# Kernel tuning notes

Hardware: AMD Instinct MI355X
Metric: run time of the kernel (lower is better)

Reference implementation:

```python
import jax, jax.numpy as jnp
import numpy as np

N, E, D, ED = 50000, 800000, 64, 2


def setup_inputs() -> dict:
    key = jax.random.key(0)
    ks = jax.random.split(key, 16)
    inp = {
        "h": jax.random.normal(ks[0], (N, D), jnp.float32),
        "coord": jax.random.normal(ks[1], (N, 3), jnp.float32),
        "edge_index": jax.random.randint(ks[2], (2, E), 0, N, jnp.int32),
        "edge_attr": jax.random.normal(ks[3], (E, ED), jnp.float32),
        # edge_mlp: Linear(2D+1+ED -> D), Linear(D -> D)
        "W_e1": jax.random.normal(ks[4], (2 * D + 1 + ED, D), jnp.float32) * 0.08,
        "b_e1": jnp.zeros((D,), jnp.float32),
        "W_e2": jax.random.normal(ks[5], (D, D), jnp.float32) * 0.12,
        "b_e2": jnp.zeros((D,), jnp.float32),
        # node_mlp: Linear(D+D -> D), Linear(D -> D)
        "W_n1": jax.random.normal(ks[6], (2 * D, D), jnp.float32) * 0.08,
        "b_n1": jnp.zeros((D,), jnp.float32),
        "W_n2": jax.random.normal(ks[7], (D, D), jnp.float32) * 0.12,
        "b_n2": jnp.zeros((D,), jnp.float32),
        # coord_mlp: Linear(D -> D), Linear(D -> 1, bias=False, xavier gain 0.001)
        "W_c1": jax.random.normal(ks[8], (D, D), jnp.float32) * 0.12,
        "b_c1": jnp.zeros((D,), jnp.float32),
        "W_c2": jax.random.normal(ks[9], (D, 1), jnp.float32) * 1e-3,
    }
    return inp


def reference(h, coord, edge_index, edge_attr,
              W_e1, b_e1, W_e2, b_e2,
              W_n1, b_n1, W_n2, b_n2,
              W_c1, b_c1, W_c2):
    row, col = edge_index[0], edge_index[1]
    n_nodes = h.shape[0]

    # coord2radial
    coord_diff = coord[row] - coord[col]                       # [E,3]
    radial = jnp.sum(coord_diff * coord_diff, axis=-1, keepdims=True)  # [E,1]

    # edge_model
    e_in = jnp.concatenate([h[row], h[col], radial, edge_attr], axis=-1)  # [E, 2D+1+ED]
    e = jax.nn.silu(e_in @ W_e1 + b_e1)
    edge_feat = jax.nn.silu(e @ W_e2 + b_e2)                   # [E,D]

    # coord_model: trans = coord_diff * coord_mlp(edge_feat), clamp, segment mean
    scale = jax.nn.silu(edge_feat @ W_c1 + b_c1) @ W_c2        # [E,1]
    trans = jnp.clip(coord_diff * scale, -100.0, 100.0)        # [E,3]
    agg_c = jax.ops.segment_sum(trans, row, num_segments=n_nodes)       # [N,3]
    cnt = jax.ops.segment_sum(jnp.ones((trans.shape[0],), trans.dtype), row,
                              num_segments=n_nodes)            # [N]
    coord_out = coord + agg_c / jnp.clip(cnt, 1.0, None)[:, None]  # coords_weight=1.0

    # node_model: segment sum of edge_feat by row, node MLP, residual
    agg_h = jax.ops.segment_sum(edge_feat, row, num_segments=n_nodes)   # [N,D]
    n_in = jnp.concatenate([h, agg_h], axis=-1)                # [N,2D]
    h_out = h + (jax.nn.silu(n_in @ W_n1 + b_n1) @ W_n2 + b_n2)

    return (h_out, coord_out)
```

## Files before the change

kernel.cpp:

```cpp
#include <hip/hip_runtime.h>

#define DD 64
#define NTE 512
#define SLOTMAX 64

using s8v   = __attribute__((ext_vector_type(8))) short;
using f32x4 = __attribute__((ext_vector_type(4))) float;

typedef unsigned int   uint_t;
typedef unsigned short ushort_t;

union U8 { s8v v; uint_t u[4]; };

__device__ __forceinline__ float silu_f(float x) {
    return x / (1.0f + __expf(-x));
}
__device__ __forceinline__ float clamp100(float x) {
    return fminf(fmaxf(x, -100.0f), 100.0f);
}
__device__ __forceinline__ unsigned short f2bf(float x) {
    unsigned int u = __float_as_uint(x);
    return (unsigned short)((u + 0x7FFFu + ((u >> 16) & 1u)) >> 16);
}
__device__ __forceinline__ uint_t cvt_pk_bf16(float lo, float hi) {
    uint_t r;
    asm("v_cvt_pk_bf16_f32 %0, %1, %2" : "=v"(r) : "v"(lo), "v"(hi));
    return r;
}

#define WAVE_FENCE() do { asm volatile("s_waitcnt lgkmcnt(0)" ::: "memory"); \
                          __builtin_amdgcn_sched_barrier(0); } while (0)

__global__ __launch_bounds__(256) void prep_all(
    const float* __restrict__ h,
    const float* __restrict__ coord,
    const float* __restrict__ We1, const float* __restrict__ We2,
    const float* __restrict__ Wc1,
    const float* __restrict__ Wn1, const float* __restrict__ Wn2,
    const float* __restrict__ be1, const float* __restrict__ be2,
    const float* __restrict__ bc1,
    const int*   __restrict__ ei,
    ushort_t* __restrict__ hbf,
    ushort_t* __restrict__ wf,
    float4* __restrict__ coord4,
    int* __restrict__ cnt_i,
    int2* __restrict__ slots2,
    int N, int E, int total8, int histBlocks, int hbfBlocks, int c4Blocks)
{
    const int b = blockIdx.x;
    if (b < histBlocks) {
        const int e = b * 256 + threadIdx.x;
        if (e < E) {
            const int r = ei[e];
            const int s = atomicAdd(&cnt_i[r], 1);
            if (s < SLOTMAX) {
                int2 v; v.x = e; v.y = ei[E + e];
                slots2[(size_t)r * SLOTMAX + s] = v;
            }
        }
    } else if (b < histBlocks + hbfBlocks) {
        const int t = (b - histBlocks) * 256 + threadIdx.x;
        if (t < total8) {
            const float4 v0 = ((const float4*)h)[t * 2 + 0];
            const float4 v1 = ((const float4*)h)[t * 2 + 1];
            uint4 o;
            o.x = (uint_t)f2bf(v0.x) | ((uint_t)f2bf(v0.y) << 16);
            o.y = (uint_t)f2bf(v0.z) | ((uint_t)f2bf(v0.w) << 16);
            o.z = (uint_t)f2bf(v1.x) | ((uint_t)f2bf(v1.y) << 16);
            o.w = (uint_t)f2bf(v1.z) | ((uint_t)f2bf(v1.w) << 16);
            ((uint4*)hbf)[t] = o;
        }
    } else if (b < histBlocks + hbfBlocks + c4Blocks) {
        const int t = (b - histBlocks - hbfBlocks) * 256 + threadIdx.x;
        if (t < N) {
            float4 c;
            c.x = coord[3 * t + 0];
            c.y = coord[3 * t + 1];
            c.z = coord[3 * t + 2];
            c.w = 0.0f;
            coord4[t] = c;
        }
    } else {
        const int t = (b - histBlocks - hbfBlocks - c4Blocks) * 256 + threadIdx.x;
        if (t >= 32768) return;
        if (t < 28672) {
            const int j    = t & 7;
            const int lane = (t >> 3) & 63;
            const int n0   = (t >> 9) & 3;
            const int k0   = (t >> 11) & 1;
            const int mat  = t >> 12;
            const int g    = lane >> 4;
            int k;
            if (mat == 2 || mat == 3) k = 16 * (2 * k0 + (j >> 2)) + 4 * g + (j & 3);
            else                      k = k0 * 32 + g * 8 + j;
            const int n = n0 * 16 + (lane & 15);
            float v;
            if      (mat == 0) v = We1[(size_t)k * 64 + n];
            else if (mat == 1) v = We1[(size_t)(64 + k) * 64 + n];
            else if (mat == 2) v = We2[(size_t)k * 64 + n];
            else if (mat == 3) v = Wc1[(size_t)k * 64 + n];
            else if (mat == 4) v = Wn1[(size_t)k * 64 + n];
            else if (mat == 5) v = Wn1[(size_t)(64 + k) * 64 + n];
            else               v = Wn2[(size_t)k * 64 + n];
            wf[t] = f2bf(v);
        } else {
            const int t2   = t - 28672;
            const int j    = t2 & 7;
            const int lane = (t2 >> 3) & 63;
            const int n0   = (t2 >> 9) & 3;
            const int xm   = (t2 >> 11) & 1;
            const int k = 8 * (lane >> 4) + j;
            const int m = n0 * 16 + (lane & 15);
            float v = 0.0f;
            if (xm == 0) {
                if      (k == 0) v = We1[(size_t)128 * 64 + m];
                else if (k == 1) v = We1[(size_t)129 * 64 + m];
                else if (k == 2) v = We1[(size_t)130 * 64 + m];
                else if (k == 3) v = be1[m];
            } else {
                if      (k == 0) v = be2[m];
                else if (k == 1) v = bc1[m];
            }
            wf[t] = f2bf(v);
        }
    }
}

__global__ __launch_bounds__(NTE, 4) void egcl_edge(
    const ushort_t* __restrict__ hbf,
    const ushort_t* __restrict__ wfG,
    const float4* __restrict__ coord4,
    const float* __restrict__ ea,
    const float* __restrict__ Wc2,
    const int* __restrict__ cnt_i,
    const int2* __restrict__ slots2,
    ushort_t* __restrict__ aggbf,
    float* __restrict__ coord_out,
    int N, int totalWaves)
{
    __shared__ ushort_t fragLDS[20480];

    const int tid = threadIdx.x;
    #pragma unroll
    for (int i = 0; i < 4; ++i)
        ((uint4*)fragLDS)[tid + i * 512] = ((const uint4*)wfG)[tid + i * 512];
    ((uint4*)fragLDS)[2048 + tid] = ((const uint4*)wfG)[3584 + tid];
    __syncthreads();

    const int wid  = tid >> 6;
    const int lane = tid & 63;
    const int l15  = lane & 15;
    const int g    = lane >> 4;

#define LD_W(mat, k0, m0) \
    (*(const s8v*)(fragLDS + ((((mat)*2 + (k0))*4 + (m0)) * 512) + lane * 8))
#define LD_X7(m0) (*(const s8v*)(fragLDS + 16384 + (m0) * 512 + lane * 8))
#define LD_XB(m0) (*(const s8v*)(fragLDS + 18432 + (m0) * 512 + lane * 8))

    float wc2_c[4][4];
    #pragma unroll
    for (int m0 = 0; m0 < 4; ++m0)
        #pragma unroll
        for (int j = 0; j < 4; ++j)
            wc2_c[m0][j] = Wc2[m0 * 16 + 4 * g + j];

    U8 b2f, bcf;
    b2f.u[0] = 0x00003F80u; b2f.u[1] = 0; b2f.u[2] = 0; b2f.u[3] = 0;
    bcf.u[0] = 0x3F800000u; bcf.u[1] = 0; bcf.u[2] = 0; bcf.u[3] = 0;

    const f32x4 zero4 = {0.f, 0.f, 0.f, 0.f};

    int n = blockIdx.x * 8 + wid;
    int pdeg = 0;
    int2 pslot; pslot.x = 0; pslot.y = 0;
    if (n < N) {
        pdeg  = cnt_i[n];
        pslot = slots2[(size_t)n * SLOTMAX + l15];
    }

    for (; n < N; n += totalWaves) {
        const int deg    = pdeg;
        const int2 slot0 = pslot;
        const int nn = n + totalWaves;
        if (nn < N) {
            pdeg  = cnt_i[nn];
            pslot = slots2[(size_t)nn * SLOTMAX + l15];
        }

        const int effdeg = deg < SLOTMAX ? deg : SLOTMAX;
        const float4 cn4 = coord4[n];
        const int s0x = __shfl(slot0.x, lane & 48, 64);
        const int s0y = __shfl(slot0.y, lane & 48, 64);

        const ushort_t* hn = hbf + (size_t)n * 64;
        const s8v bn0 = *(const s8v*)(hn + g * 8);
        const s8v bn1 = *(const s8v*)(hn + 32 + g * 8);
        f32x4 rowacc[4];
        #pragma unroll
        for (int m0 = 0; m0 < 4; ++m0) {
            f32x4 a = zero4;
            a = __builtin_amdgcn_mfma_f32_16x16x32_bf16(LD_W(0, 0, m0), bn0, a, 0, 0, 0);
            a = __builtin_amdgcn_mfma_f32_16x16x32_bf16(LD_W(0, 1, m0), bn1, a, 0, 0, 0);
            rowacc[m0] = a;
        }

        float hsum[4][4];
        #pragma unroll
        for (int m0 = 0; m0 < 4; ++m0)
            #pragma unroll
            for (int j = 0; j < 4; ++j) hsum[m0][j] = 0.f;
        float txs = 0.f, tys = 0.f, tzs = 0.f;

        const int ntile = (effdeg + 15) >> 4;
        int2 slNext; slNext.x = 0; slNext.y = 0;

        for (int t = 0; t < ntile; ++t) {
            const int s = t * 16 + l15;
            const bool val = (s < effdeg);
            const float valf = val ? 1.0f : 0.0f;

            int2 sl;
            if (t == 0) { sl.x = val ? slot0.x : s0x; sl.y = val ? slot0.y : s0y; }
            else        sl = slNext;

            if (t + 1 < ntile) {
                const int s2 = s + 16;
                slNext = slots2[(size_t)n * SLOTMAX + (s2 < effdeg ? s2 : 0)];
            }

            const float4 c4 = coord4[sl.y];
            const float2 a2 = *(const float2*)(ea + 2 * (size_t)sl.x);
            const ushort_t* hc = hbf + (size_t)sl.y * 64;
            const s8v bc0  = *(const s8v*)(hc + g * 8);
            const s8v bc1v = *(const s8v*)(hc + 32 + g * 8);

            const float dx = cn4.x - c4.x, dy = cn4.y - c4.y, dz = cn4.z - c4.z;
            const float radial = dx * dx + dy * dy + dz * dz;

            U8 ex;
            ex.u[0] = cvt_pk_bf16(radial, a2.x);
            ex.u[1] = cvt_pk_bf16(a2.y, 1.0f);
            ex.u[2] = 0; ex.u[3] = 0;

            f32x4 c1[4];
            #pragma unroll
            for (int m0 = 0; m0 < 4; ++m0) {
                f32x4 a = rowacc[m0];
                a = __builtin_amdgcn_mfma_f32_16x16x32_bf16(LD_W(1, 0, m0), bc0,  a, 0, 0, 0);
                a = __builtin_amdgcn_mfma_f32_16x16x32_bf16(LD_W(1, 1, m0), bc1v, a, 0, 0, 0);
                a = __builtin_amdgcn_mfma_f32_16x16x32_bf16(LD_X7(m0),      ex.v, a, 0, 0, 0);
                c1[m0] = a;
            }

            U8 f2a, f2b;
            #pragma unroll
            for (int m0 = 0; m0 < 4; ++m0) {
                const float ya = silu_f(c1[m0][0]);
                const float yb = silu_f(c1[m0][1]);
                const float yc = silu_f(c1[m0][2]);
                const float yd = silu_f(c1[m0][3]);
                U8& dst = (m0 < 2) ? f2a : f2b;
                dst.u[(m0 & 1) * 2 + 0] = cvt_pk_bf16(ya, yb);
                dst.u[(m0 & 1) * 2 + 1] = cvt_pk_bf16(yc, yd);
            }

            f32x4 c2[4];
            #pragma unroll
            for (int m0 = 0; m0 < 4; ++m0) {
                f32x4 a = zero4;
                a = __builtin_amdgcn_mfma_f32_16x16x32_bf16(LD_W(2, 0, m0), f2a.v, a, 0, 0, 0);
                a = __builtin_amdgcn_mfma_f32_16x16x32_bf16(LD_W(2, 1, m0), f2b.v, a, 0, 0, 0);
                a = __builtin_amdgcn_mfma_f32_16x16x32_bf16(LD_XB(m0),      b2f.v, a, 0, 0, 0);
                c2[m0] = a;
            }

            U8 f3a, f3b;
            #pragma unroll
            for (int m0 = 0; m0 < 4; ++m0) {
                const float ya = silu_f(c2[m0][0]);
                const float yb = silu_f(c2[m0][1]);
                const float yc = silu_f(c2[m0][2]);
                const float yd = silu_f(c2[m0][3]);
                hsum[m0][0] = fmaf(ya, valf, hsum[m0][0]);
                hsum[m0][1] = fmaf(yb, valf, hsum[m0][1]);
                hsum[m0][2] = fmaf(yc, valf, hsum[m0][2]);
                hsum[m0][3] = fmaf(yd, valf, hsum[m0][3]);
                U8& dst = (m0 < 2) ? f3a : f3b;
                dst.u[(m0 & 1) * 2 + 0] = cvt_pk_bf16(ya, yb);
                dst.u[(m0 & 1) * 2 + 1] = cvt_pk_bf16(yc, yd);
            }

            float p = 0.f;
            #pragma unroll
            for (int m0 = 0; m0 < 4; ++m0) {
                f32x4 a = zero4;
                a = __builtin_amdgcn_mfma_f32_16x16x32_bf16(LD_W(3, 0, m0), f3a.v, a, 0, 0, 0);
                a = __builtin_amdgcn_mfma_f32_16x16x32_bf16(LD_W(3, 1, m0), f3b.v, a, 0, 0, 0);
                a = __builtin_amdgcn_mfma_f32_16x16x32_bf16(LD_XB(m0),      bcf.v, a, 0, 0, 0);
                #pragma unroll
                for (int j = 0; j < 4; ++j)
                    p = fmaf(silu_f(a[j]), wc2_c[m0][j], p);
            }
            p += __shfl_xor(p, 16, 64);
            p += __shfl_xor(p, 32, 64);
            const float sc = p * valf;
            txs += clamp100(dx * sc);
            tys += clamp100(dy * sc);
            tzs += clamp100(dz * sc);
        }

        #pragma unroll
        for (int m0 = 0; m0 < 4; ++m0) {
            #pragma unroll
            for (int j = 0; j < 4; ++j) {
                float v = hsum[m0][j];
                v += __shfl_xor(v, 1, 64);
                v += __shfl_xor(v, 2, 64);
                v += __shfl_xor(v, 4, 64);
                v += __shfl_xor(v, 8, 64);
                hsum[m0][j] = v;
            }
        }
        if (l15 == 0) {
            uint_t* ab = (uint_t*)aggbf + (size_t)n * 32 + 2 * g;
            #pragma unroll
            for (int m0 = 0; m0 < 4; ++m0) {
                ab[8 * m0 + 0] = cvt_pk_bf16(hsum[m0][0], hsum[m0][1]);
                ab[8 * m0 + 1] = cvt_pk_bf16(hsum[m0][2], hsum[m0][3]);
            }
        }
        #pragma unroll
        for (int msk = 1; msk < 64; msk <<= 1) {
            txs += __shfl_xor(txs, msk, 64);
            tys += __shfl_xor(tys, msk, 64);
            tzs += __shfl_xor(tzs, msk, 64);
        }
        if (lane == 0) {
            const float inv = 0.25f / fmaxf((float)deg, 1.0f);
            coord_out[(size_t)n * 3 + 0] = cn4.x + txs * inv;
            coord_out[(size_t)n * 3 + 1] = cn4.y + tys * inv;
            coord_out[(size_t)n * 3 + 2] = cn4.z + tzs * inv;
        }
    }
#undef LD_W
#undef LD_X7
#undef LD_XB
}

__global__ __launch_bounds__(NTE, 4) void egcl_node(
    const ushort_t* __restrict__ hbf,
    const ushort_t* __restrict__ aggbf,
    const ushort_t* __restrict__ wfG,
    const float* __restrict__ h,
    const float* __restrict__ bn1,
    const float* __restrict__ bn2,
    float* __restrict__ h_out,
    int N)
{
    __shared__ ushort_t fragLDS[12288];
    __shared__ ushort_t ldsY[8][16 * 72];

    const int tid = threadIdx.x;
    #pragma unroll
    for (int i = 0; i < 3; ++i)
        ((uint4*)fragLDS)[tid + i * 512] = ((const uint4*)(wfG + 16384))[tid + i * 512];
    __syncthreads();

    const int wid  = tid >> 6;
    const int lane = tid & 63;
    const int l15  = lane & 15;
    const int g    = lane >> 4;

#define LD_WN(mat, k0, n0) \
    (*(const s8v*)(fragLDS + ((((mat)*2 + (k0))*4 + (n0)) * 512) + lane * 8))

    float bn1_c[4], bn2_c[4];
    #pragma unroll
    for (int n0 = 0; n0 < 4; ++n0) {
        bn1_c[n0] = bn1[n0 * 16 + l15];
        bn2_c[n0] = bn2[n0 * 16 + l15];
    }

    const int wg = blockIdx.x * 8 + wid;
    const int nb = wg * 16;
    if (nb >= N) return;

    const int nod  = nb + l15;
    const int nodL = nod < N ? nod : N - 1;
    const ushort_t* hrow = hbf   + (size_t)nodL * 64;
    const ushort_t* arow = aggbf + (size_t)nodL * 64;
    const s8v aH0 = *(const s8v*)(hrow + g * 8);
    const s8v aH1 = *(const s8v*)(hrow + 32 + g * 8);
    const s8v aG0 = *(const s8v*)(arow + g * 8);
    const s8v aG1 = *(const s8v*)(arow + 32 + g * 8);

    ushort_t* yw = ldsY[wid];
    #pragma unroll
    for (int n0 = 0; n0 < 4; ++n0) {
        f32x4 a = {0.f, 0.f, 0.f, 0.f};
        a = __builtin_amdgcn_mfma_f32_16x16x32_bf16(aH0, LD_WN(0, 0, n0), a, 0, 0, 0);
        a = __builtin_amdgcn_mfma_f32_16x16x32_bf16(aH1, LD_WN(0, 1, n0), a, 0, 0, 0);
        a = __builtin_amdgcn_mfma_f32_16x16x32_bf16(aG0, LD_WN(1, 0, n0), a, 0, 0, 0);
        a = __builtin_amdgcn_mfma_f32_16x16x32_bf16(aG1, LD_WN(1, 1, n0), a, 0, 0, 0);
        #pragma unroll
        for (int jj = 0; jj < 4; ++jj)
            yw[(g * 4 + jj) * 72 + n0 * 16 + l15] = f2bf(silu_f(a[jj] + bn1_c[n0]));
    }
    WAVE_FENCE();

    const ushort_t* yrow = yw + l15 * 72;
    const s8v b0 = *(const s8v*)(yrow + g * 8);
    const s8v b1 = *(const s8v*)(yrow + 32 + g * 8);
    #pragma unroll
    for (int n0 = 0; n0 < 4; ++n0) {
        f32x4 a = {0.f, 0.f, 0.f, 0.f};
        a = __builtin_amdgcn_mfma_f32_16x16x32_bf16(b0, LD_WN(2, 0, n0), a, 0, 0, 0);
        a = __builtin_amdgcn_mfma_f32_16x16x32_bf16(b1, LD_WN(2, 1, n0), a, 0, 0, 0);
        #pragma unroll
        for (int jj = 0; jj < 4; ++jj) {
            const int m = nb + g * 4 + jj;
            if (m < N) {
                const size_t idx = (size_t)m * 64 + n0 * 16 + l15;
                h_out[idx] = h[idx] + (a[jj] + bn2_c[n0]);
            }
        }
    }
#undef LD_WN
}

extern "C" void kernel_launch(void* const* d_in, const int* in_sizes, int n_in,
                              void* d_out, int out_size, void* d_ws, size_t ws_size,
                              hipStream_t stream) {
    const float* h     = (const float*)d_in[0];
    const float* coord = (const float*)d_in[1];
    const int*   ei    = (const int*)  d_in[2];
    const float* ea    = (const float*)d_in[3];
    const float* We1   = (const float*)d_in[4];
    const float* be1   = (const float*)d_in[5];
    const float* We2   = (const float*)d_in[6];
    const float* be2   = (const float*)d_in[7];
    const float* Wn1   = (const float*)d_in[8];
    const float* bn1   = (const float*)d_in[9];
    const float* Wn2   = (const float*)d_in[10];
    const float* bn2   = (const float*)d_in[11];
    const float* Wc1   = (const float*)d_in[12];
    const float* bc1   = (const float*)d_in[13];
    const float* Wc2   = (const float*)d_in[14];

    const int N = in_sizes[0] / DD;
    const int E = in_sizes[3] / 2;

    float* out       = (float*)d_out;
    float* h_out     = out;
    float* coord_out = out + (size_t)N * DD;

    char* base = (char*)d_ws;
    ushort_t* hbf   = (ushort_t*)base;
    const size_t o_wf    = (size_t)N * DD * 2;
    ushort_t* wf    = (ushort_t*)(base + o_wf);
    const size_t o_agg   = o_wf + 32768 * 2;
    ushort_t* aggbf = (ushort_t*)(base + o_agg);
    const size_t o_c4    = o_agg + (size_t)N * DD * 2;
    float4* coord4  = (float4*)(base + o_c4);
    const size_t o_cnt   = o_c4 + (size_t)N * 16;
    int* cnt_i      = (int*)(base + o_cnt);
    const size_t o_slots = o_cnt + (size_t)N * 4;
    int2* slots2    = (int2*)(base + o_slots);

    hipMemsetAsync((void*)cnt_i, 0, (size_t)N * 4, stream);

    const int histBlocks = (E + 255) / 256;
    const int total8     = N * DD / 8;
    const int hbfBlocks  = (total8 + 255) / 256;
    const int c4Blocks   = (N + 255) / 256;
    const int wfBlocks   = (32768 + 255) / 256;
    prep_all<<<histBlocks + hbfBlocks + c4Blocks + wfBlocks, 256, 0, stream>>>(
        h, coord, We1, We2, Wc1, Wn1, Wn2, be1, be2, bc1, ei,
        hbf, wf, coord4, cnt_i, slots2, N, E, total8,
        histBlocks, hbfBlocks, c4Blocks);

    const int eblocks = 1024;
    const int totalWaves = eblocks * 8;
    egcl_edge<<<eblocks, NTE, 0, stream>>>(
        hbf, wf, coord4, ea, Wc2,
        cnt_i, slots2, aggbf, coord_out, N, totalWaves);

    const int nwaves  = (N + 15) / 16;
    const int nblocks = (nwaves + 7) / 8;
    egcl_node<<<nblocks, NTE, 0, stream>>>(
        hbf, aggbf, wf, h, bn1, bn2, h_out, N);
}
```

Baseline: 255.1 us.

## Software-pipeline neighbor gathers and shrink edge kernel blocks to 256 threads

The edge kernel now loads all 64 slot entries per node up front, one per lane, and distributes neighbor indices with shuffles instead of reloading slots for each tile. It prefetches the next tile's neighbor coordinates, edge attributes and bf16 features, and the next node's own features and coordinates, so gather latency overlaps the MFMA work of the current tile. Blocks shrink to 256 threads (4 waves), with twice as many blocks and launch bounds changed to (256,3). The aim is to hide global-memory latency, at the cost of more registers for the prefetched values and a 40 KB LDS weight copy per block, which is now shared by fewer waves.

```diff
diff --git a/kernel.cpp b/kernel.cpp
--- a/kernel.cpp
+++ b/kernel.cpp
@@ -126,7 +126,7 @@
     }
 }
 
-__global__ __launch_bounds__(NTE, 4) void egcl_edge(
+__global__ __launch_bounds__(256, 3) void egcl_edge(
     const ushort_t* __restrict__ hbf,
     const ushort_t* __restrict__ wfG,
     const float4* __restrict__ coord4,
@@ -142,9 +142,10 @@
 
     const int tid = threadIdx.x;
     #pragma unroll
-    for (int i = 0; i < 4; ++i)
-        ((uint4*)fragLDS)[tid + i * 512] = ((const uint4*)wfG)[tid + i * 512];
-    ((uint4*)fragLDS)[2048 + tid] = ((const uint4*)wfG)[3584 + tid];
+    for (int i = 0; i < 8; ++i)
+        ((uint4*)fragLDS)[tid + i * 256] = ((const uint4*)wfG)[tid + i * 256];
+    ((uint4*)fragLDS)[2048 + tid]       = ((const uint4*)wfG)[3584 + tid];
+    ((uint4*)fragLDS)[2048 + 256 + tid] = ((const uint4*)wfG)[3584 + 256 + tid];
     __syncthreads();
 
     const int wid  = tid >> 6;
@@ -170,31 +171,53 @@
 
     const f32x4 zero4 = {0.f, 0.f, 0.f, 0.f};
 
-    int n = blockIdx.x * 8 + wid;
-    int pdeg = 0;
-    int2 pslot; pslot.x = 0; pslot.y = 0;
+    int n = blockIdx.x * 4 + wid;
+
+    int    pdeg = 0;
+    int2   pslot; pslot.x = 0; pslot.y = 0;
+    s8v    phn0{}, phn1{};
+    float4 pcn4{};
     if (n < N) {
         pdeg  = cnt_i[n];
-        pslot = slots2[(size_t)n * SLOTMAX + l15];
+        pslot = slots2[(size_t)n * SLOTMAX + lane];
+        const ushort_t* hn = hbf + (size_t)n * 64;
+        phn0 = *(const s8v*)(hn + g * 8);
+        phn1 = *(const s8v*)(hn + 32 + g * 8);
+        pcn4 = coord4[n];
     }
 
     for (; n < N; n += totalWaves) {
-        const int deg    = pdeg;
-        const int2 slot0 = pslot;
+        const int    deg    = pdeg;
+        const int2   myslot = pslot;
+        const s8v    bn0    = phn0;
+        const s8v    bn1    = phn1;
+        const float4 cn4    = pcn4;
+
         const int nn = n + totalWaves;
         if (nn < N) {
             pdeg  = cnt_i[nn];
-            pslot = slots2[(size_t)nn * SLOTMAX + l15];
+            pslot = slots2[(size_t)nn * SLOTMAX + lane];
+            const ushort_t* hn2 = hbf + (size_t)nn * 64;
+            phn0 = *(const s8v*)(hn2 + g * 8);
+            phn1 = *(const s8v*)(hn2 + 32 + g * 8);
+            pcn4 = coord4[nn];
         }
 
         const int effdeg = deg < SLOTMAX ? deg : SLOTMAX;
-        const float4 cn4 = coord4[n];
-        const int s0x = __shfl(slot0.x, lane & 48, 64);
-        const int s0y = __shfl(slot0.y, lane & 48, 64);
-
-        const ushort_t* hn = hbf + (size_t)n * 64;
-        const s8v bn0 = *(const s8v*)(hn + g * 8);
-        const s8v bn1 = *(const s8v*)(hn + 32 + g * 8);
+        const int ntile  = (effdeg + 15) >> 4;
+
+        float4 c4c{}; float2 a2c{}; s8v bc0c{}, bc1c{};
+        if (ntile > 0) {
+            const int si = (l15 < effdeg) ? l15 : 0;
+            const int ec = __shfl(myslot.x, si, 64);
+            const int cc = __shfl(myslot.y, si, 64);
+            c4c = coord4[cc];
+            a2c = *(const float2*)(ea + 2 * (size_t)ec);
+            const ushort_t* hc = hbf + (size_t)cc * 64;
+            bc0c = *(const s8v*)(hc + g * 8);
+            bc1c = *(const s8v*)(hc + 32 + g * 8);
+        }
+
         f32x4 rowacc[4];
         #pragma unroll
         for (int m0 = 0; m0 < 4; ++m0) {
@@ -211,43 +234,40 @@
             for (int j = 0; j < 4; ++j) hsum[m0][j] = 0.f;
         float txs = 0.f, tys = 0.f, tzs = 0.f;
 
-        const int ntile = (effdeg + 15) >> 4;
-        int2 slNext; slNext.x = 0; slNext.y = 0;
-
         for (int t = 0; t < ntile; ++t) {
             const int s = t * 16 + l15;
             const bool val = (s < effdeg);
             const float valf = val ? 1.0f : 0.0f;
 
-            int2 sl;
-            if (t == 0) { sl.x = val ? slot0.x : s0x; sl.y = val ? slot0.y : s0y; }
-            else        sl = slNext;
-
-            if (t + 1 < ntile) {
+            float4 c4n{}; float2 a2n{}; s8v bc0n{}, bc1n{};
+            {
                 const int s2 = s + 16;
-                slNext = slots2[(size_t)n * SLOTMAX + (s2 < effdeg ? s2 : 0)];
-            }
-
-            const float4 c4 = coord4[sl.y];
-            const float2 a2 = *(const float2*)(ea + 2 * (size_t)sl.x);
-            const ushort_t* hc = hbf + (size_t)sl.y * 64;
-            const s8v bc0  = *(const s8v*)(hc + g * 8);
-            const s8v bc1v = *(const s8v*)(hc + 32 + g * 8);
-
-            const float dx = cn4.x - c4.x, dy = cn4.y - c4.y, dz = cn4.z - c4.z;
+                const int si = (s2 < effdeg) ? s2 : 0;
+                const int en = __shfl(myslot.x, si, 64);
+                const int cn = __shfl(myslot.y, si, 64);
+                if (t + 1 < ntile) {
+                    c4n = coord4[cn];
+                    a2n = *(const float2*)(ea + 2 * (size_t)en);
+                    const ushort_t* hc2 = hbf + (size_t)cn * 64;
+                    bc0n = *(const s8v*)(hc2 + g * 8);
+                    bc1n = *(const s8v*)(hc2 + 32 + g * 8);
+                }
+            }
+
+            const float dx = cn4.x - c4c.x, dy = cn4.y - c4c.y, dz = cn4.z - c4c.z;
             const float radial = dx * dx + dy * dy + dz * dz;
 
             U8 ex;
-            ex.u[0] = cvt_pk_bf16(radial, a2.x);
-            ex.u[1] = cvt_pk_bf16(a2.y, 1.0f);
+            ex.u[0] = cvt_pk_bf16(radial, a2c.x);
+            ex.u[1] = cvt_pk_bf16(a2c.y, 1.0f);
             ex.u[2] = 0; ex.u[3] = 0;
 
             f32x4 c1[4];
             #pragma unroll
             for (int m0 = 0; m0 < 4; ++m0) {
                 f32x4 a = rowacc[m0];
-                a = __builtin_amdgcn_mfma_f32_16x16x32_bf16(LD_W(1, 0, m0), bc0,  a, 0, 0, 0);
-                a = __builtin_amdgcn_mfma_f32_16x16x32_bf16(LD_W(1, 1, m0), bc1v, a, 0, 0, 0);
+                a = __builtin_amdgcn_mfma_f32_16x16x32_bf16(LD_W(1, 0, m0), bc0c, a, 0, 0, 0);
+                a = __builtin_amdgcn_mfma_f32_16x16x32_bf16(LD_W(1, 1, m0), bc1c, a, 0, 0, 0);
                 a = __builtin_amdgcn_mfma_f32_16x16x32_bf16(LD_X7(m0),      ex.v, a, 0, 0, 0);
                 c1[m0] = a;
             }
@@ -307,6 +327,10 @@
             txs += clamp100(dx * sc);
             tys += clamp100(dy * sc);
             tzs += clamp100(dz * sc);
+
+            if (t + 1 < ntile) {
+                c4c = c4n; a2c = a2n; bc0c = bc0n; bc1c = bc1n;
+            }
         }
 
         #pragma unroll
@@ -479,9 +503,9 @@
         hbf, wf, coord4, cnt_i, slots2, N, E, total8,
         histBlocks, hbfBlocks, c4Blocks);
 
-    const int eblocks = 1024;
-    const int totalWaves = eblocks * 8;
-    egcl_edge<<<eblocks, NTE, 0, stream>>>(
+    const int eblocks = 2048;
+    const int totalWaves = eblocks * 4;
+    egcl_edge<<<eblocks, 256, 0, stream>>>(
         hbf, wf, coord4, ea, Wc2,
         cnt_i, slots2, aggbf, coord_out, N, totalWaves);
 
```

Result: slower. 262.3 us (+2.8%).

## Split edge kernel into per-edge MLP pass and separate gather-aggregate kernel

Applied to the files above, without the earlier changes.

Replaces the node-centric edge kernel, which walked each node's slot list in 16-edge tiles, with an edge-parallel kernel that processes contiguous 16-edge tiles and writes edge features (bf16) and clamped coordinate translations to workspace. A new aggregation kernel then gathers those per-edge results through the slot lists to form agg_h and coord_out. This removes the per-node padding waste and degree-dependent load imbalance, and the slot lists now store only edge ids. In exchange it adds a round trip of roughly 100 MB of bf16 edge features plus the trans buffer through memory, an extra launch, and the row-side layer-1 MFMAs are now redone for every edge instead of once per node.

```diff
diff --git a/kernel.cpp b/kernel.cpp
--- a/kernel.cpp
+++ b/kernel.cpp
@@ -1,7 +1,6 @@
 #include <hip/hip_runtime.h>
 
 #define DD 64
-#define NTE 512
 #define SLOTMAX 64
 
 using s8v   = __attribute__((ext_vector_type(8))) short;
@@ -21,6 +20,9 @@
 __device__ __forceinline__ unsigned short f2bf(float x) {
     unsigned int u = __float_as_uint(x);
     return (unsigned short)((u + 0x7FFFu + ((u >> 16) & 1u)) >> 16);
+}
+__device__ __forceinline__ float bf2f(ushort_t v) {
+    return __uint_as_float(((uint_t)v) << 16);
 }
 __device__ __forceinline__ uint_t cvt_pk_bf16(float lo, float hi) {
     uint_t r;
@@ -44,7 +46,7 @@
     ushort_t* __restrict__ wf,
     float4* __restrict__ coord4,
     int* __restrict__ cnt_i,
-    int2* __restrict__ slots2,
+    int* __restrict__ slots,
     int N, int E, int total8, int histBlocks, int hbfBlocks, int c4Blocks)
 {
     const int b = blockIdx.x;
@@ -53,10 +55,7 @@
         if (e < E) {
             const int r = ei[e];
             const int s = atomicAdd(&cnt_i[r], 1);
-            if (s < SLOTMAX) {
-                int2 v; v.x = e; v.y = ei[E + e];
-                slots2[(size_t)r * SLOTMAX + s] = v;
-            }
+            if (s < SLOTMAX) slots[(size_t)r * SLOTMAX + s] = e;
         }
     } else if (b < histBlocks + hbfBlocks) {
         const int t = (b - histBlocks) * 256 + threadIdx.x;
@@ -126,17 +125,16 @@
     }
 }
 
-__global__ __launch_bounds__(NTE, 4) void egcl_edge(
+__global__ __launch_bounds__(512, 4) void egcl_edge(
     const ushort_t* __restrict__ hbf,
     const ushort_t* __restrict__ wfG,
     const float4* __restrict__ coord4,
+    const int*   __restrict__ ei,
     const float* __restrict__ ea,
     const float* __restrict__ Wc2,
-    const int* __restrict__ cnt_i,
-    const int2* __restrict__ slots2,
-    ushort_t* __restrict__ aggbf,
-    float* __restrict__ coord_out,
-    int N, int totalWaves)
+    uint_t* __restrict__ efu,
+    float4* __restrict__ trans4,
+    int E, int ntiles, int totalWaves)
 {
     __shared__ ushort_t fragLDS[20480];
 
@@ -170,176 +168,105 @@
 
     const f32x4 zero4 = {0.f, 0.f, 0.f, 0.f};
 
-    int n = blockIdx.x * 8 + wid;
-    int pdeg = 0;
-    int2 pslot; pslot.x = 0; pslot.y = 0;
-    if (n < N) {
-        pdeg  = cnt_i[n];
-        pslot = slots2[(size_t)n * SLOTMAX + l15];
-    }
-
-    for (; n < N; n += totalWaves) {
-        const int deg    = pdeg;
-        const int2 slot0 = pslot;
-        const int nn = n + totalWaves;
-        if (nn < N) {
-            pdeg  = cnt_i[nn];
-            pslot = slots2[(size_t)nn * SLOTMAX + l15];
-        }
-
-        const int effdeg = deg < SLOTMAX ? deg : SLOTMAX;
-        const float4 cn4 = coord4[n];
-        const int s0x = __shfl(slot0.x, lane & 48, 64);
-        const int s0y = __shfl(slot0.y, lane & 48, 64);
-
-        const ushort_t* hn = hbf + (size_t)n * 64;
-        const s8v bn0 = *(const s8v*)(hn + g * 8);
-        const s8v bn1 = *(const s8v*)(hn + 32 + g * 8);
-        f32x4 rowacc[4];
+    for (int t = blockIdx.x * 8 + wid; t < ntiles; t += totalWaves) {
+        const int e   = t * 16 + l15;
+        const bool val = (e < E);
+        const int eL  = val ? e : (E - 1);
+
+        const int row = ei[eL];
+        const int col = ei[E + eL];
+        const float4 cr = coord4[row];
+        const float4 cc = coord4[col];
+        const float2 a2 = *(const float2*)(ea + 2 * (size_t)eL);
+        const ushort_t* hr = hbf + (size_t)row * 64;
+        const ushort_t* hc = hbf + (size_t)col * 64;
+        const s8v br0 = *(const s8v*)(hr + g * 8);
+        const s8v br1 = *(const s8v*)(hr + 32 + g * 8);
+        const s8v bc0 = *(const s8v*)(hc + g * 8);
+        const s8v bc1 = *(const s8v*)(hc + 32 + g * 8);
+
+        const float dx = cr.x - cc.x, dy = cr.y - cc.y, dz = cr.z - cc.z;
+        const float radial = dx * dx + dy * dy + dz * dz;
+
+        U8 ex;
+        ex.u[0] = cvt_pk_bf16(radial, a2.x);
+        ex.u[1] = cvt_pk_bf16(a2.y, 1.0f);
+        ex.u[2] = 0; ex.u[3] = 0;
+
+        f32x4 c1[4];
         #pragma unroll
         for (int m0 = 0; m0 < 4; ++m0) {
             f32x4 a = zero4;
-            a = __builtin_amdgcn_mfma_f32_16x16x32_bf16(LD_W(0, 0, m0), bn0, a, 0, 0, 0);
-            a = __builtin_amdgcn_mfma_f32_16x16x32_bf16(LD_W(0, 1, m0), bn1, a, 0, 0, 0);
-            rowacc[m0] = a;
-        }
-
-        float hsum[4][4];
-        #pragma unroll
-        for (int m0 = 0; m0 < 4; ++m0)
+            a = __builtin_amdgcn_mfma_f32_16x16x32_bf16(LD_W(0, 0, m0), br0, a, 0, 0, 0);
+            a = __builtin_amdgcn_mfma_f32_16x16x32_bf16(LD_W(0, 1, m0), br1, a, 0, 0, 0);
+            a = __builtin_amdgcn_mfma_f32_16x16x32_bf16(LD_W(1, 0, m0), bc0, a, 0, 0, 0);
+            a = __builtin_amdgcn_mfma_f32_16x16x32_bf16(LD_W(1, 1, m0), bc1, a, 0, 0, 0);
+            a = __builtin_amdgcn_mfma_f32_16x16x32_bf16(LD_X7(m0),      ex.v, a, 0, 0, 0);
+            c1[m0] = a;
+        }
+
+        U8 f2a, f2b;
+        #pragma unroll
+        for (int m0 = 0; m0 < 4; ++m0) {
+            const float ya = silu_f(c1[m0][0]);
+            const float yb = silu_f(c1[m0][1]);
+            const float yc = silu_f(c1[m0][2]);
+            const float yd = silu_f(c1[m0][3]);
+            U8& dst = (m0 < 2) ? f2a : f2b;
+            dst.u[(m0 & 1) * 2 + 0] = cvt_pk_bf16(ya, yb);
+            dst.u[(m0 & 1) * 2 + 1] = cvt_pk_bf16(yc, yd);
+        }
+
+        f32x4 c2[4];
+        #pragma unroll
+        for (int m0 = 0; m0 < 4; ++m0) {
+            f32x4 a = zero4;
+            a = __builtin_amdgcn_mfma_f32_16x16x32_bf16(LD_W(2, 0, m0), f2a.v, a, 0, 0, 0);
+            a = __builtin_amdgcn_mfma_f32_16x16x32_bf16(LD_W(2, 1, m0), f2b.v, a, 0, 0, 0);
+            a = __builtin_amdgcn_mfma_f32_16x16x32_bf16(LD_XB(m0),      b2f.v, a, 0, 0, 0);
+            c2[m0] = a;
+        }
+
+        uint_t* efrow = efu + (size_t)e * 32;
+        U8 f3a, f3b;
+        #pragma unroll
+        for (int m0 = 0; m0 < 4; ++m0) {
+            const float ya = silu_f(c2[m0][0]);
+            const float yb = silu_f(c2[m0][1]);
+            const float yc = silu_f(c2[m0][2]);
+            const float yd = silu_f(c2[m0][3]);
+            const uint_t p0 = cvt_pk_bf16(ya, yb);
+            const uint_t p1 = cvt_pk_bf16(yc, yd);
+            U8& dst = (m0 < 2) ? f3a : f3b;
+            dst.u[(m0 & 1) * 2 + 0] = p0;
+            dst.u[(m0 & 1) * 2 + 1] = p1;
+            if (val) {
+                uint2 st; st.x = p0; st.y = p1;
+                *(uint2*)(efrow + m0 * 8 + g * 2) = st;
+            }
+        }
+
+        float p = 0.f;
+        #pragma unroll
+        for (int m0 = 0; m0 < 4; ++m0) {
+            f32x4 a = zero4;
+            a = __builtin_amdgcn_mfma_f32_16x16x32_bf16(LD_W(3, 0, m0), f3a.v, a, 0, 0, 0);
+            a = __builtin_amdgcn_mfma_f32_16x16x32_bf16(LD_W(3, 1, m0), f3b.v, a, 0, 0, 0);
+            a = __builtin_amdgcn_mfma_f32_16x16x32_bf16(LD_XB(m0),      bcf.v, a, 0, 0, 0);
             #pragma unroll
-            for (int j = 0; j < 4; ++j) hsum[m0][j] = 0.f;
-        float txs = 0.f, tys = 0.f, tzs = 0.f;
-
-        const int ntile = (effdeg + 15) >> 4;
-        int2 slNext; slNext.x = 0; slNext.y = 0;
-
-        for (int t = 0; t < ntile; ++t) {
-            const int s = t * 16 + l15;
-            const bool val = (s < effdeg);
-            const float valf = val ? 1.0f : 0.0f;
-
-            int2 sl;
-            if (t == 0) { sl.x = val ? slot0.x : s0x; sl.y = val ? slot0.y : s0y; }
-            else        sl = slNext;
-
-            if (t + 1 < ntile) {
-                const int s2 = s + 16;
-                slNext = slots2[(size_t)n * SLOTMAX + (s2 < effdeg ? s2 : 0)];
-            }
-
-            const float4 c4 = coord4[sl.y];
-            const float2 a2 = *(const float2*)(ea + 2 * (size_t)sl.x);
-            const ushort_t* hc = hbf + (size_t)sl.y * 64;
-            const s8v bc0  = *(const s8v*)(hc + g * 8);
-            const s8v bc1v = *(const s8v*)(hc + 32 + g * 8);
-
-            const float dx = cn4.x - c4.x, dy = cn4.y - c4.y, dz = cn4.z - c4.z;
-            const float radial = dx * dx + dy * dy + dz * dz;
-
-            U8 ex;
-            ex.u[0] = cvt_pk_bf16(radial, a2.x);
-            ex.u[1] = cvt_pk_bf16(a2.y, 1.0f);
-            ex.u[2] = 0; ex.u[3] = 0;
-
-            f32x4 c1[4];
-            #pragma unroll
-            for (int m0 = 0; m0 < 4; ++m0) {
-                f32x4 a = rowacc[m0];
-                a = __builtin_amdgcn_mfma_f32_16x16x32_bf16(LD_W(1, 0, m0), bc0,  a, 0, 0, 0);
-                a = __builtin_amdgcn_mfma_f32_16x16x32_bf16(LD_W(1, 1, m0), bc1v, a, 0, 0, 0);
-                a = __builtin_amdgcn_mfma_f32_16x16x32_bf16(LD_X7(m0),      ex.v, a, 0, 0, 0);
-                c1[m0] = a;
-            }
-
-            U8 f2a, f2b;
-            #pragma unroll
-            for (int m0 = 0; m0 < 4; ++m0) {
-                const float ya = silu_f(c1[m0][0]);
-                const float yb = silu_f(c1[m0][1]);
-                const float yc = silu_f(c1[m0][2]);
-                const float yd = silu_f(c1[m0][3]);
-                U8& dst = (m0 < 2) ? f2a : f2b;
-                dst.u[(m0 & 1) * 2 + 0] = cvt_pk_bf16(ya, yb);
-                dst.u[(m0 & 1) * 2 + 1] = cvt_pk_bf16(yc, yd);
-            }
-
-            f32x4 c2[4];
-            #pragma unroll
-            for (int m0 = 0; m0 < 4; ++m0) {
-                f32x4 a = zero4;
-                a = __builtin_amdgcn_mfma_f32_16x16x32_bf16(LD_W(2, 0, m0), f2a.v, a, 0, 0, 0);
-                a = __builtin_amdgcn_mfma_f32_16x16x32_bf16(LD_W(2, 1, m0), f2b.v, a, 0, 0, 0);
-                a = __builtin_amdgcn_mfma_f32_16x16x32_bf16(LD_XB(m0),      b2f.v, a, 0, 0, 0);
-                c2[m0] = a;
-            }
-
-            U8 f3a, f3b;
-            #pragma unroll
-            for (int m0 = 0; m0 < 4; ++m0) {
-                const float ya = silu_f(c2[m0][0]);
-                const float yb = silu_f(c2[m0][1]);
-                const float yc = silu_f(c2[m0][2]);
-                const float yd = silu_f(c2[m0][3]);
-                hsum[m0][0] = fmaf(ya, valf, hsum[m0][0]);
-                hsum[m0][1] = fmaf(yb, valf, hsum[m0][1]);
-                hsum[m0][2] = fmaf(yc, valf, hsum[m0][2]);
-                hsum[m0][3] = fmaf(yd, valf, hsum[m0][3]);
-                U8& dst = (m0 < 2) ? f3a : f3b;
-                dst.u[(m0 & 1) * 2 + 0] = cvt_pk_bf16(ya, yb);
-                dst.u[(m0 & 1) * 2 + 1] = cvt_pk_bf16(yc, yd);
-            }
-
-            float p = 0.f;
-            #pragma unroll
-            for (int m0 = 0; m0 < 4; ++m0) {
-                f32x4 a = zero4;
-                a = __builtin_amdgcn_mfma_f32_16x16x32_bf16(LD_W(3, 0, m0), f3a.v, a, 0, 0, 0);
-                a = __builtin_amdgcn_mfma_f32_16x16x32_bf16(LD_W(3, 1, m0), f3b.v, a, 0, 0, 0);
-                a = __builtin_amdgcn_mfma_f32_16x16x32_bf16(LD_XB(m0),      bcf.v, a, 0, 0, 0);
-                #pragma unroll
-                for (int j = 0; j < 4; ++j)
-                    p = fmaf(silu_f(a[j]), wc2_c[m0][j], p);
-            }
-            p += __shfl_xor(p, 16, 64);
-            p += __shfl_xor(p, 32, 64);
-            const float sc = p * valf;
-            txs += clamp100(dx * sc);
-            tys += clamp100(dy * sc);
-            tzs += clamp100(dz * sc);
-        }
-
-        #pragma unroll
-        for (int m0 = 0; m0 < 4; ++m0) {
-            #pragma unroll
-            for (int j = 0; j < 4; ++j) {
-                float v = hsum[m0][j];
-                v += __shfl_xor(v, 1, 64);
-                v += __shfl_xor(v, 2, 64);
-                v += __shfl_xor(v, 4, 64);
-                v += __shfl_xor(v, 8, 64);
-                hsum[m0][j] = v;
-            }
-        }
-        if (l15 == 0) {
-            uint_t* ab = (uint_t*)aggbf + (size_t)n * 32 + 2 * g;
-            #pragma unroll
-            for (int m0 = 0; m0 < 4; ++m0) {
-                ab[8 * m0 + 0] = cvt_pk_bf16(hsum[m0][0], hsum[m0][1]);
-                ab[8 * m0 + 1] = cvt_pk_bf16(hsum[m0][2], hsum[m0][3]);
-            }
-        }
-        #pragma unroll
-        for (int msk = 1; msk < 64; msk <<= 1) {
-            txs += __shfl_xor(txs, msk, 64);
-            tys += __shfl_xor(tys, msk, 64);
-            tzs += __shfl_xor(tzs, msk, 64);
-        }
-        if (lane == 0) {
-            const float inv = 0.25f / fmaxf((float)deg, 1.0f);
-            coord_out[(size_t)n * 3 + 0] = cn4.x + txs * inv;
-            coord_out[(size_t)n * 3 + 1] = cn4.y + tys * inv;
-            coord_out[(size_t)n * 3 + 2] = cn4.z + tzs * inv;
+            for (int j = 0; j < 4; ++j)
+                p = fmaf(silu_f(a[j]), wc2_c[m0][j], p);
+        }
+        p += __shfl_xor(p, 16, 64);
+        p += __shfl_xor(p, 32, 64);
+
+        if (val && g == 0) {
+            float4 tr;
+            tr.x = clamp100(dx * p);
+            tr.y = clamp100(dy * p);
+            tr.z = clamp100(dz * p);
+            tr.w = 1.0f;
+            trans4[e] = tr;
         }
     }
 #undef LD_W
@@ -347,7 +274,59 @@
 #undef LD_XB
 }
 
-__global__ __launch_bounds__(NTE, 4) void egcl_node(
+__global__ __launch_bounds__(256) void egcl_agg(
+    const ushort_t* __restrict__ efbf,
+    const float4* __restrict__ trans4,
+    const int* __restrict__ slots,
+    const int* __restrict__ cnt_i,
+    const float4* __restrict__ coord4,
+    ushort_t* __restrict__ aggbf,
+    float* __restrict__ coord_out,
+    int N)
+{
+    const int wid  = threadIdx.x >> 6;
+    const int lane = threadIdx.x & 63;
+    const int n = blockIdx.x * 4 + wid;
+    if (n >= N) return;
+
+    const int deg = cnt_i[n];
+    const int eff = deg < SLOTMAX ? deg : SLOTMAX;
+    const int* sp = slots + (size_t)n * SLOTMAX;
+
+    float a0 = 0.f, a1 = 0.f, a2 = 0.f, a3 = 0.f;
+    float tx = 0.f, ty = 0.f, tz = 0.f;
+
+    int s = 0;
+    for (; s + 4 <= eff; s += 4) {
+        const int e0 = sp[s], e1 = sp[s + 1], e2 = sp[s + 2], e3 = sp[s + 3];
+        const float4 t0 = trans4[e0], t1 = trans4[e1], t2 = trans4[e2], t3 = trans4[e3];
+        const ushort_t v0 = efbf[(size_t)e0 * 64 + lane];
+        const ushort_t v1 = efbf[(size_t)e1 * 64 + lane];
+        const ushort_t v2 = efbf[(size_t)e2 * 64 + lane];
+        const ushort_t v3 = efbf[(size_t)e3 * 64 + lane];
+        a0 += bf2f(v0); a1 += bf2f(v1); a2 += bf2f(v2); a3 += bf2f(v3);
+        tx += t0.x + t1.x + t2.x + t3.x;
+        ty += t0.y + t1.y + t2.y + t3.y;
+        tz += t0.z + t1.z + t2.z + t3.z;
+    }
+    for (; s < eff; ++s) {
+        const int e0 = sp[s];
+        a0 += bf2f(efbf[(size_t)e0 * 64 + lane]);
+        const float4 t0 = trans4[e0];
+        tx += t0.x; ty += t0.y; tz += t0.z;
+    }
+
+    aggbf[(size_t)n * 64 + lane] = f2bf(a0 + a1 + a2 + a3);
+    if (lane == 0) {
+        const float inv = 1.0f / fmaxf((float)deg, 1.0f);
+        const float4 cn = coord4[n];
+        coord_out[(size_t)n * 3 + 0] = cn.x + tx * inv;
+        coord_out[(size_t)n * 3 + 1] = cn.y + ty * inv;
+        coord_out[(size_t)n * 3 + 2] = cn.z + tz * inv;
+    }
+}
+
+__global__ __launch_bounds__(512, 4) void egcl_node(
     const ushort_t* __restrict__ hbf,
     const ushort_t* __restrict__ aggbf,
     const ushort_t* __restrict__ wfG,
@@ -465,7 +444,11 @@
     const size_t o_cnt   = o_c4 + (size_t)N * 16;
     int* cnt_i      = (int*)(base + o_cnt);
     const size_t o_slots = o_cnt + (size_t)N * 4;
-    int2* slots2    = (int2*)(base + o_slots);
+    int* slots      = (int*)(base + o_slots);
+    const size_t o_tr    = o_slots + (size_t)N * SLOTMAX * 4;
+    float4* trans4  = (float4*)(base + o_tr);
+    const size_t o_ef    = o_tr + (size_t)E * 16;
+    ushort_t* efbf  = (ushort_t*)(base + o_ef);
 
     hipMemsetAsync((void*)cnt_i, 0, (size_t)N * 4, stream);
 
@@ -476,17 +459,22 @@
     const int wfBlocks   = (32768 + 255) / 256;
     prep_all<<<histBlocks + hbfBlocks + c4Blocks + wfBlocks, 256, 0, stream>>>(
         h, coord, We1, We2, Wc1, Wn1, Wn2, be1, be2, bc1, ei,
-        hbf, wf, coord4, cnt_i, slots2, N, E, total8,
+        hbf, wf, coord4, cnt_i, slots, N, E, total8,
         histBlocks, hbfBlocks, c4Blocks);
 
+    const int ntiles = (E + 15) / 16;
     const int eblocks = 1024;
     const int totalWaves = eblocks * 8;
-    egcl_edge<<<eblocks, NTE, 0, stream>>>(
-        hbf, wf, coord4, ea, Wc2,
-        cnt_i, slots2, aggbf, coord_out, N, totalWaves);
+    egcl_edge<<<eblocks, 512, 0, stream>>>(
+        hbf, wf, coord4, ei, ea, Wc2,
+        (uint_t*)efbf, trans4, E, ntiles, totalWaves);
+
+    const int ablocks = (N + 3) / 4;
+    egcl_agg<<<ablocks, 256, 0, stream>>>(
+        efbf, trans4, slots, cnt_i, coord4, aggbf, coord_out, N);
 
     const int nwaves  = (N + 15) / 16;
     const int nblocks = (nwaves + 7) / 8;
-    egcl_node<<<nblocks, NTE, 0, stream>>>(
+    egcl_node<<<nblocks, 512, 0, stream>>>(
         hbf, aggbf, wf, h, bn1, bn2, h_out, N);
 }
```

Result: faster. 218.8 us (median of 2 runs) (-14.2%).
